# Kernel optimization log

Hardware: AMD Instinct MI355X
Metric: run time of the kernel (lower is better)

Reference implementation:

```python
import jax, jax.numpy as jnp
import numpy as np

SLOPE = 0.01  # LeakyReLU default negative slope
EPS = 1e-5    # BatchNorm eps


def _lrelu(x):
    return jnp.where(x >= 0, x, SLOPE * x)


def _conv(x, w, b):
    # x: [B,C,H,W], w: [O,I,kh,kw] (torch layout)
    y = jax.lax.conv_general_dilated(x, w, (1, 1), 'VALID',
                                     dimension_numbers=('NCHW', 'OIHW', 'NCHW'))
    return y + b[None, :, None, None]


def _bn4(x, p):
    # eval-mode BatchNorm2d; p = [gamma, beta, running_mean, running_var] stacked [4,C]
    g, b, m, v = p
    s = g * jax.lax.rsqrt(v + EPS)
    return x * s[None, :, None, None] + (b - m * s)[None, :, None, None]


def _forward(observation, action, sc1_w, sc1_b, sbn1, sc2_w, sc2_b, sbn2,
             mc1_w, mc1_b, mbn1, mc2_w, mc2_b, mbn2,
             gw_root, gw_rel, g_b, gbn,
             a_cw, a_cb, a_w1, a_b1, a_w2, a_b2, a_w3, a_b3,
             edge_index, edge_type, nodes_to_select):
    # ---- multi-scale temporal CNN (eval mode: dropout = identity) ----
    s = _lrelu(_bn4(_conv(observation, sc1_w, sc1_b), sbn1))
    s = _lrelu(_bn4(_conv(s, sc2_w, sc2_b), sbn2))          # [B,20,N,1]
    m = _lrelu(_bn4(_conv(observation, mc1_w, mc1_b), mbn1))
    m = _lrelu(_bn4(_conv(m, mc2_w, mc2_b), mbn2))          # [B,20,N,1]
    l = _lrelu(jnp.max(observation, axis=3, keepdims=True)) # [B,3,N,1]
    temporal = jnp.concatenate([s, m, l], axis=1)           # [B,43,N,1]

    # ---- RGCN (graph replicated per batch element; aggr='mean' per relation) ----
    x = jnp.swapaxes(temporal[..., 0], 1, 2)                # [B,N,F]
    N = x.shape[1]
    src, dst = edge_index[0], edge_index[1]
    out = jnp.einsum('bnf,fg->bng', x, gw_root) + g_b       # root transform + bias
    for r in range(gw_rel.shape[0]):
        h = jnp.einsum('bnf,fg->bng', x, gw_rel[r])         # per-relation transform
        mask = (edge_type == r).astype(x.dtype)             # [E]
        msgs = h[:, src, :] * mask[None, :, None]           # [B,E,F] gather
        agg = jax.ops.segment_sum(jnp.swapaxes(msgs, 0, 1), dst, num_segments=N)  # [N,B,F]
        deg = jax.ops.segment_sum(mask, dst, num_segments=N)                       # [N]
        out = out + jnp.swapaxes(agg, 0, 1) / jnp.maximum(deg, 1.0)[None, :, None]
    # BatchNorm1d (eval) + LeakyReLU; dropout = identity
    g, be, mu, v = gbn
    sg = g * jax.lax.rsqrt(v + EPS)
    out = _lrelu(out * sg + (be - mu * sg))                 # [B,N,F]

    graph_feats = jnp.swapaxes(out, 1, 2)[..., None]        # [B,F,N,1]
    feats = jnp.concatenate([temporal, graph_feats], axis=1)  # [B,86,N,1]
    feats = feats[:, :, nodes_to_select, :]                 # [B,86,P,1]

    # ---- actor head (mode == 'actor'); cash_bias is zeroed in the original ----
    stocks = action[:, 1:][:, None, :, None]                # [B,1,P,1]
    f = jnp.concatenate([stocks, feats], axis=1)[..., 0]    # [B,87,P]
    logits = jnp.einsum('bcp,c->bp', f, a_cw) + a_cb[0]     # 1x1 conv, out_ch=1
    o = jnp.concatenate([jnp.zeros((f.shape[0], 1), f.dtype), logits], axis=1)  # [B,P+1]
    h1 = jax.nn.relu(o @ a_w1 + a_b1)
    h2 = jax.nn.relu(h1 @ a_w2 + a_b2)
    return jax.nn.softmax(h2 @ a_w3 + a_b3, axis=-1)


def setup_inputs() -> dict:
    key = jax.random.key(0)
    ks = jax.random.split(key, 30)
    B, C0, N, T = 64, 3, 500, 50
    E, R, P, H = 16000, 4, 500, 128
    CM, CF = 3, 20
    F = 2 * CF + C0  # 43

    def rn(k, sh, s=0.1):
        return jax.random.normal(k, sh, jnp.float32) * s

    def bn_p(k, c):
        k1, k2, k3, k4 = jax.random.split(k, 4)
        return jnp.stack([jax.random.uniform(k1, (c,), jnp.float32, 0.5, 1.5),
                          rn(k2, (c,)), rn(k3, (c,)),
                          jax.random.uniform(k4, (c,), jnp.float32, 0.5, 1.5)])

    return {
        'observation': jax.random.normal(ks[0], (B, C0, N, T), jnp.float32),
        'action': jax.random.uniform(ks[1], (B, P + 1), jnp.float32),
        'edge_index': jax.random.randint(ks[2], (2, E), 0, N),
        'edge_type': jax.random.randint(ks[3], (E,), 0, R),
        'nodes_to_select': jnp.arange(P),
        'sc1_w': rn(ks[4], (CM, C0, 1, 3)), 'sc1_b': rn(ks[5], (CM,)), 'sbn1': bn_p(ks[6], CM),
        'sc2_w': rn(ks[7], (CF, CM, 1, 48)), 'sc2_b': rn(ks[8], (CF,)), 'sbn2': bn_p(ks[9], CF),
        'mc1_w': rn(ks[10], (CM, C0, 1, 21)), 'mc1_b': rn(ks[11], (CM,)), 'mbn1': bn_p(ks[12], CM),
        'mc2_w': rn(ks[13], (CF, CM, 1, 30)), 'mc2_b': rn(ks[14], (CF,)), 'mbn2': bn_p(ks[15], CF),
        'gw_root': rn(ks[16], (F, F)), 'gw_rel': rn(ks[17], (R, F, F)),
        'g_b': rn(ks[18], (F,)), 'gbn': bn_p(ks[19], F),
        'a_cw': rn(ks[20], (2 * F + 1,)), 'a_cb': rn(ks[21], (1,)),
        'a_w1': rn(ks[22], (P + 1, H)), 'a_b1': rn(ks[23], (H,)),
        'a_w2': rn(ks[24], (H, H)), 'a_b2': rn(ks[25], (H,)),
        'a_w3': rn(ks[26], (H, P + 1)), 'a_b3': rn(ks[27], (P + 1,)),
    }


def reference(observation, action, edge_index, edge_type, nodes_to_select,
              sc1_w, sc1_b, sbn1, sc2_w, sc2_b, sbn2,
              mc1_w, mc1_b, mbn1, mc2_w, mc2_b, mbn2,
              gw_root, gw_rel, g_b, gbn,
              a_cw, a_cb, a_w1, a_b1, a_w2, a_b2, a_w3, a_b3):
    return _forward(observation, action, sc1_w, sc1_b, sbn1, sc2_w, sc2_b, sbn2,
                    mc1_w, mc1_b, mbn1, mc2_w, mc2_b, mbn2,
                    gw_root, gw_rel, g_b, gbn,
                    a_cw, a_cb, a_w1, a_b1, a_w2, a_b2, a_w3, a_b3,
                    edge_index, edge_type, nodes_to_select)
```

## Files before the change

### kernel.cpp

```cpp
#include <hip/hip_runtime.h>

#define SLOPE 0.01f
#define EPSV  1e-5f
#define BB    64
#define NN    500
#define TT    50
#define E_N   16000
#define FF    43
#define PP    500
#define HH    128
#define XSTRIDE 48
#define PAD_E 40

typedef const float* fp;

__device__ __forceinline__ float lrelu(float x){ return x >= 0.f ? x : SLOPE * x; }
__device__ __forceinline__ float bnap(float x, fp bnp, int c, int C){
  float g  = bnp[c], b_ = bnp[C + c];
  float m  = bnp[2*C + c], v = bnp[3*C + c];
  float s = g * rsqrtf(v + EPSV);
  return x * s + (b_ - m * s);
}

#define DPP_I(x, c) __builtin_amdgcn_update_dpp(0, (x), (c), 0xF, 0xF, true)
__device__ __forceinline__ float rsum16(float x){
  x += __int_as_float(DPP_I(__float_as_int(x), 0xB1));
  x += __int_as_float(DPP_I(__float_as_int(x), 0x4E));
  x += __int_as_float(DPP_I(__float_as_int(x), 0x124));
  x += __int_as_float(DPP_I(__float_as_int(x), 0x128));
  return x;
}
__device__ __forceinline__ float rmax16(float x){
  x = fmaxf(x, __int_as_float(DPP_I(__float_as_int(x), 0xB1)));
  x = fmaxf(x, __int_as_float(DPP_I(__float_as_int(x), 0x4E)));
  x = fmaxf(x, __int_as_float(DPP_I(__float_as_int(x), 0x124)));
  x = fmaxf(x, __int_as_float(DPP_I(__float_as_int(x), 0x128)));
  return x;
}

__global__ __launch_bounds__(512) void k_tempo24(
    fp obs, fp sc1w, fp mc1w, fp sc2w, fp mc2w,
    fp sc1b, fp sbn1, fp sc2b, fp sbn2,
    fp mc1b, fp mbn1, fp mc2b, fp mbn2,
    const int* __restrict__ ei, const int* __restrict__ et,
    int* __restrict__ cntg, int* __restrict__ esp,
    float* __restrict__ xbuf)
{
  __shared__ float OL[4896];
  __shared__ float WSr[2880];
  __shared__ float WMr[1800];
  __shared__ float TBL[100];
  int tid  = threadIdx.x;
  int w    = tid >> 6, lane = tid & 63;
  int node = lane >> 4, seg = lane & 15;
  int gg   = __builtin_amdgcn_readfirstlane(blockIdx.x*8 + w);
  int b    = gg / 125, ng = gg - b*125;
  int n0   = ng * 4;
  int wbase = w * 612;

  for (int i = tid; i < 720; i += 512) *(float4*)(WSr + i*4) = *(const float4*)(sc2w + i*4);
  for (int i = tid; i < 450; i += 512) *(float4*)(WMr + i*4) = *(const float4*)(mc2w + i*4);

  if (tid < 20){
    float g = sbn2[tid], b_ = sbn2[20+tid], m = sbn2[40+tid], v = sbn2[60+tid];
    float s = g * rsqrtf(v + EPSV);
    TBL[tid] = s; TBL[43+tid] = sc2b[tid]*s + (b_ - m*s);
  } else if (tid < 40){
    int o = tid - 20;
    float g = mbn2[o], b_ = mbn2[20+o], m = mbn2[40+o], v = mbn2[60+o];
    float s = g * rsqrtf(v + EPSV);
    TBL[tid] = s; TBL[43+tid] = mc2b[o]*s + (b_ - m*s);
  } else if (tid < 43){
    TBL[tid] = 1.f; TBL[43+tid] = 0.f;
  } else if (tid < 46){
    int ci = tid - 43;
    float g = sbn1[ci], b_ = sbn1[3+ci], m = sbn1[6+ci], v = sbn1[9+ci];
    float s = g * rsqrtf(v + EPSV);
    TBL[86+ci] = s; TBL[89+ci] = sc1b[ci]*s + (b_ - m*s);
  } else if (tid < 49){
    int ci = tid - 46;
    float g = mbn1[ci], b_ = mbn1[3+ci], m = mbn1[6+ci], v = mbn1[9+ci];
    float s = g * rsqrtf(v + EPSV);
    TBL[92+ci] = s; TBL[95+ci] = mc1b[ci]*s + (b_ - m*s);
  }

  if (blockIdx.x < 8){
    int base = blockIdx.x * 2000;
    #pragma unroll
    for (int k = 0; k < 4; k++){
      int el = k*512 + tid;
      if (el < 2000){
        int e = base + el;
        int s = ei[e], d = ei[E_N + e], r = et[e];
        int idx = d*4 + r;
        int pos = atomicAdd(&cntg[idx], 1);
        if (pos < PAD_E) esp[idx*PAD_E + pos] = s;
      }
    }
  }

  for (int c = 0; c < 3; c++){
    if (lane < 50){
      const float4 v = *(const float4*)(obs + ((size_t)(b*3+c)*NN + n0)*TT + lane*4);
      int f = lane*4;
      int n = f/50, t = f - n*50;
      int a = wbase + c*204 + n*51 + t;
      OL[a] = v.x;
      if (++t == 50){ t = 0; n++; a = wbase + c*204 + n*51; } else a++;
      OL[a] = v.y;
      if (++t == 50){ t = 0; n++; a = wbase + c*204 + n*51; } else a++;
      OL[a] = v.z;
      if (++t == 50){ t = 0; n++; a = wbase + c*204 + n*51; } else a++;
      OL[a] = v.w;
    }
  }
  __syncthreads();

  int rb = wbase + node*51;
  int g  = b*NN + n0 + node;
  float* xr = xbuf + (size_t)g * XSTRIDE;
  float acc[20];

  {
    float mv[3][3];
    #pragma unroll
    for (int i = 0; i < 3; i++)
      #pragma unroll
      for (int co = 0; co < 3; co++) mv[i][co] = 0.f;
    int t0 = seg*3;
    #pragma unroll
    for (int ci = 0; ci < 3; ci++){
      int ab = rb + ci*204 + t0;
      float v0 = OL[ab], v1 = OL[ab+1], v2 = OL[ab+2], v3 = OL[ab+3], v4 = OL[ab+4];
      #pragma unroll
      for (int co = 0; co < 3; co++){
        float w0 = sc1w[co*9+ci*3+0], w1 = sc1w[co*9+ci*3+1], w2 = sc1w[co*9+ci*3+2];
        mv[0][co] += v0*w0 + v1*w1 + v2*w2;
        mv[1][co] += v1*w0 + v2*w1 + v3*w2;
        mv[2][co] += v2*w0 + v3*w1 + v4*w2;
      }
    }
    #pragma unroll
    for (int o = 0; o < 20; o++) acc[o] = 0.f;
    #pragma unroll
    for (int i = 0; i < 3; i++){
      int tt = t0 + i;
      #pragma unroll
      for (int co = 0; co < 3; co++){
        float z = lrelu(mv[i][co]*TBL[86+co] + TBL[89+co]);
        const float* wr = WSr + co*48 + tt;
        #pragma unroll
        for (int o = 0; o < 20; o++)
          acc[o] += z * wr[o*144];
      }
    }
    #pragma unroll
    for (int o = 0; o < 20; o++) acc[o] = rsum16(acc[o]);
    #pragma unroll
    for (int o = 0; o < 20; o++)
      if (seg == (o & 15)) xr[o] = lrelu(acc[o]*TBL[o] + TBL[43+o]);
  }

  {
    float mv[2][3];
    #pragma unroll
    for (int i = 0; i < 2; i++)
      #pragma unroll
      for (int co = 0; co < 3; co++) mv[i][co] = 0.f;
    int t0 = seg*2;
    #pragma unroll
    for (int ci = 0; ci < 3; ci++){
      int ab = rb + ci*204 + t0;
      float vc = OL[ab];
      #pragma unroll
      for (int k = 0; k < 21; k++){
        float vn = OL[ab + k + 1];
        #pragma unroll
        for (int co = 0; co < 3; co++){
          float wk = mc1w[co*63 + ci*21 + k];
          mv[0][co] += vc*wk;
          mv[1][co] += vn*wk;
        }
        vc = vn;
      }
    }
    #pragma unroll
    for (int o = 0; o < 20; o++) acc[o] = 0.f;
    if (seg < 15){
      #pragma unroll
      for (int co = 0; co < 3; co++){
        float z0 = lrelu(mv[0][co]*TBL[92+co] + TBL[95+co]);
        float z1 = lrelu(mv[1][co]*TBL[92+co] + TBL[95+co]);
        const float* wr = WMr + co*30 + t0;
        #pragma unroll
        for (int o = 0; o < 20; o++){
          float2 q = *(const float2*)(wr + o*90);
          acc[o] += z0*q.x + z1*q.y;
        }
      }
    }
    #pragma unroll
    for (int o = 0; o < 20; o++) acc[o] = rsum16(acc[o]);
    #pragma unroll
    for (int o = 0; o < 20; o++)
      if (seg == (o & 15)) xr[20+o] = lrelu(acc[o]*TBL[20+o] + TBL[63+o]);
  }

  {
    float m0 = -3e38f, m1 = -3e38f, m2 = -3e38f;
    int l0 = seg*4;
    int ln = 50 - l0; if (ln > 4) ln = 4;
    for (int j = 0; j < ln; j++){
      m0 = fmaxf(m0, OL[rb +       l0 + j]);
      m1 = fmaxf(m1, OL[rb + 204 + l0 + j]);
      m2 = fmaxf(m2, OL[rb + 408 + l0 + j]);
    }
    m0 = rmax16(m0); m1 = rmax16(m1); m2 = rmax16(m2);
    if (seg == 0) xr[40] = lrelu(m0);
    if (seg == 1) xr[41] = lrelu(m1);
    if (seg == 2) xr[42] = lrelu(m2);
  }
}

__global__ __launch_bounds__(1024) void k_graph17(
    const float* __restrict__ xbuf,
    fp gwroot, fp gwrel, fp gb, fp gbnp,
    const int* __restrict__ cntg, const int* __restrict__ esp,
    fp action, fp acw, fp acb,
    float* __restrict__ o_ws)
{
  __shared__ float xin[64][219];
  __shared__ float lred[16][64];
  int p = blockIdx.x;
  int l = ((p & 7) * 63) + (p >> 3);
  if (l >= 500) return;
  int tid = threadIdx.x;
  int w = tid >> 6, lane = tid & 63;
  int g0 = l * 64;

  for (int q = 0; q < 4; q++){
    int nl = (w << 2) + q;
    int g = __builtin_amdgcn_readfirstlane(g0 + nl);
    int b = g / NN;
    int n = g - b * NN;
    const float* xb = xbuf + (size_t)(b * NN) * XSTRIDE;
    float xv = (lane < FF) ? xbuf[(size_t)g*XSTRIDE + lane] : 0.f;
    float ar[4];
    #pragma unroll
    for (int r = 0; r < 4; r++){
      int idx = n*4 + r;
      int c = __builtin_amdgcn_readfirstlane(cntg[idx]);
      if (c > PAD_E) c = PAD_E;
      const int* ep = esp + idx*PAD_E;
      float a0 = 0.f, a1 = 0.f, a2 = 0.f, a3 = 0.f;
      int i = 0;
      for (; i + 4 <= c; i += 4){
        int s0 = ep[i], s1 = ep[i+1], s2 = ep[i+2], s3 = ep[i+3];
        float v0 = (lane < FF) ? xb[(size_t)s0*XSTRIDE + lane] : 0.f;
        float v1 = (lane < FF) ? xb[(size_t)s1*XSTRIDE + lane] : 0.f;
        float v2 = (lane < FF) ? xb[(size_t)s2*XSTRIDE + lane] : 0.f;
        float v3 = (lane < FF) ? xb[(size_t)s3*XSTRIDE + lane] : 0.f;
        a0 += v0; a1 += v1; a2 += v2; a3 += v3;
      }
      for (; i < c; i++){
        int s = ep[i];
        a0 += (lane < FF) ? xb[(size_t)s*XSTRIDE + lane] : 0.f;
      }
      ar[r] = ((a0 + a1) + (a2 + a3)) / fmaxf((float)c, 1.f);
    }
    if (lane < FF){
      xin[nl][lane]       = xv;
      xin[nl][ 43 + lane] = ar[0];
      xin[nl][ 86 + lane] = ar[1];
      xin[nl][129 + lane] = ar[2];
      xin[nl][172 + lane] = ar[3];
    }
  }
  __syncthreads();

  int c0 = __builtin_amdgcn_readfirstlane(w * 3);
  float acc[3];
  #pragma unroll
  for (int j = 0; j < 3; j++) acc[j] = (c0 + j < FF) ? gb[c0+j] : 0.f;
  for (int f = 0; f < 43; f++){
    float v = xin[lane][f];
    const float* wp = gwroot + f*43 + c0;
    #pragma unroll
    for (int j = 0; j < 3; j++) acc[j] += v * wp[j];
  }
  for (int f = 0; f < 172; f++){
    float v = xin[lane][43 + f];
    const float* wp = gwrel + f*43 + c0;
    #pragma unroll
    for (int j = 0; j < 3; j++) acc[j] += v * wp[j];
  }
  float lp = 0.f;
  #pragma unroll
  for (int j = 0; j < 3; j++){
    int c = c0 + j;
    if (c < FF){
      float gv = lrelu(bnap(acc[j], gbnp, c, FF));
      lp += gv * acw[1 + FF + c];
    }
  }
  if (w == 15){
    int g = g0 + lane;
    int b = g / NN, n = g - b * NN;
    float xp = acb[0] + action[b*(PP+1) + 1 + n] * acw[0];
    #pragma unroll 2
    for (int c = 0; c < FF; c++) xp += xin[lane][c] * acw[1 + c];
    lp = xp;
  }
  lred[w][lane] = lp;
  __syncthreads();
  if (tid < 64){
    float t = 0.f;
    #pragma unroll
    for (int w2 = 0; w2 < 16; w2++) t += lred[w2][tid];
    int g2 = g0 + tid;
    int b = g2 / NN, n = g2 - b * NN;
    o_ws[b*(PP+1) + 1 + n] = t;
  }
}

__global__ __launch_bounds__(512) void k_fcall2(
    const float* __restrict__ o_ws,
    fp aw1, fp ab1, fp aw2, fp ab2, fp aw3, fp ab3,
    float* __restrict__ out)
{
  int b = blockIdx.x;
  int tid = threadIdx.x;
  __shared__ float os[PP+1];
  __shared__ float part[4][HH];
  __shared__ float h1[HH];
  __shared__ float h2[HH];
  __shared__ float red[512];

  if (tid <= PP) os[tid] = (tid == 0) ? 0.f : o_ws[b*(PP+1) + tid];
  __syncthreads();

  {
    int chunk = tid >> 7, h = tid & 127;
    int k0 = chunk * 125;
    int kn = (chunk == 3) ? 126 : 125;
    float acc = 0.f;
    for (int k = 0; k < kn; k++) acc += os[k0+k] * aw1[(k0+k)*HH + h];
    part[chunk][h] = acc;
  }
  __syncthreads();
  if (tid < HH)
    h1[tid] = fmaxf(ab1[tid] + part[0][tid] + part[1][tid] + part[2][tid] + part[3][tid], 0.f);
  __syncthreads();
  if (tid < HH){
    float acc = ab2[tid];
    #pragma unroll 4
    for (int k = 0; k < HH; k++) acc += h1[k] * aw2[k*HH + tid];
    h2[tid] = fmaxf(acc, 0.f);
  }
  __syncthreads();

  float val = -1e30f;
  if (tid <= PP){
    float acc = ab3[tid];
    #pragma unroll 4
    for (int k = 0; k < HH; k++) acc += h2[k] * aw3[k*(PP+1) + tid];
    val = acc;
  }
  red[tid] = val;
  __syncthreads();
  for (int s = 256; s > 0; s >>= 1){
    if (tid < s) red[tid] = fmaxf(red[tid], red[tid + s]);
    __syncthreads();
  }
  float mxv = red[0];
  __syncthreads();
  float e = (tid <= PP) ? expf(val - mxv) : 0.f;
  red[tid] = e;
  __syncthreads();
  for (int s = 256; s > 0; s >>= 1){
    if (tid < s) red[tid] += red[tid + s];
    __syncthreads();
  }
  float sum = red[0];
  if (tid <= PP) out[b*(PP+1) + tid] = e / sum;
}

extern "C" void kernel_launch(void* const* d_in, const int* in_sizes, int n_in,
                              void* d_out, int out_size, void* d_ws, size_t ws_size,
                              hipStream_t stream)
{
  fp obs    = (fp)d_in[0];
  fp action = (fp)d_in[1];
  const int* ei  = (const int*)d_in[2];
  const int* et  = (const int*)d_in[3];
  fp sc1w=(fp)d_in[5],  sc1b=(fp)d_in[6],  sbn1=(fp)d_in[7];
  fp sc2w=(fp)d_in[8],  sc2b=(fp)d_in[9],  sbn2=(fp)d_in[10];
  fp mc1w=(fp)d_in[11], mc1b=(fp)d_in[12], mbn1=(fp)d_in[13];
  fp mc2w=(fp)d_in[14], mc2b=(fp)d_in[15], mbn2=(fp)d_in[16];
  fp gwroot=(fp)d_in[17], gwrel=(fp)d_in[18], gb=(fp)d_in[19], gbnp=(fp)d_in[20];
  fp acw=(fp)d_in[21], acb=(fp)d_in[22];
  fp aw1=(fp)d_in[23], ab1=(fp)d_in[24];
  fp aw2=(fp)d_in[25], ab2=(fp)d_in[26];
  fp aw3=(fp)d_in[27], ab3=(fp)d_in[28];

  float* xbuf   = (float*)d_ws;
  float* o_ws   = xbuf + 1536000;
  int*   cntg   = (int*)(o_ws + 32064);
  int*   esp    = cntg + 2000;

  float* out = (float*)d_out;

  hipMemsetAsync(cntg, 0, 2000*sizeof(int), stream);
  hipLaunchKernelGGL(k_tempo24, dim3(1000), dim3(512), 0, stream,
    obs, sc1w, mc1w, sc2w, mc2w,
    sc1b, sbn1, sc2b, sbn2, mc1b, mbn1, mc2b, mbn2,
    ei, et, cntg, esp, xbuf);
  hipLaunchKernelGGL(k_graph17, dim3(504), dim3(1024), 0, stream,
    xbuf, gwroot, gwrel, gb, gbnp, cntg, esp, action, acw, acb, o_ws);
  hipLaunchKernelGGL(k_fcall2, dim3(BB), dim3(512), 0, stream,
    o_ws, aw1, ab1, aw2, ab2, aw3, ab3, out);
}
```

Before: 226.4 us.

## Remap graph kernel blocks to one node across all batches, sharing edge lists

The RGCN aggregation kernel now assigns each block a single node index for all 64 batch elements, where before each block took 64 consecutive flattened (batch,node) rows. Each wave handles four batches and reuses every edge index load across those four batches' gathers. This cuts redundant edge-list and count reads and raises memory-level parallelism per loaded index. In exchange the gathers now stride across four separate batch slices, and the output writes to o_ws are strided by batch.

```diff
diff --git a/kernel.cpp b/kernel.cpp
--- a/kernel.cpp
+++ b/kernel.cpp
@@ -222,7 +222,7 @@
   }
 }
 
-__global__ __launch_bounds__(1024) void k_graph17(
+__global__ __launch_bounds__(1024) void k_graph20(
     const float* __restrict__ xbuf,
     fp gwroot, fp gwrel, fp gb, fp gbnp,
     const int* __restrict__ cntg, const int* __restrict__ esp,
@@ -231,49 +231,55 @@
 {
   __shared__ float xin[64][219];
   __shared__ float lred[16][64];
-  int p = blockIdx.x;
-  int l = ((p & 7) * 63) + (p >> 3);
-  if (l >= 500) return;
+  int n = blockIdx.x;
   int tid = threadIdx.x;
   int w = tid >> 6, lane = tid & 63;
-  int g0 = l * 64;
-
-  for (int q = 0; q < 4; q++){
-    int nl = (w << 2) + q;
-    int g = __builtin_amdgcn_readfirstlane(g0 + nl);
-    int b = g / NN;
-    int n = g - b * NN;
-    const float* xb = xbuf + (size_t)(b * NN) * XSTRIDE;
-    float xv = (lane < FF) ? xbuf[(size_t)g*XSTRIDE + lane] : 0.f;
-    float ar[4];
-    #pragma unroll
-    for (int r = 0; r < 4; r++){
-      int idx = n*4 + r;
-      int c = __builtin_amdgcn_readfirstlane(cntg[idx]);
-      if (c > PAD_E) c = PAD_E;
-      const int* ep = esp + idx*PAD_E;
-      float a0 = 0.f, a1 = 0.f, a2 = 0.f, a3 = 0.f;
-      int i = 0;
-      for (; i + 4 <= c; i += 4){
-        int s0 = ep[i], s1 = ep[i+1], s2 = ep[i+2], s3 = ep[i+3];
-        float v0 = (lane < FF) ? xb[(size_t)s0*XSTRIDE + lane] : 0.f;
-        float v1 = (lane < FF) ? xb[(size_t)s1*XSTRIDE + lane] : 0.f;
-        float v2 = (lane < FF) ? xb[(size_t)s2*XSTRIDE + lane] : 0.f;
-        float v3 = (lane < FF) ? xb[(size_t)s3*XSTRIDE + lane] : 0.f;
-        a0 += v0; a1 += v1; a2 += v2; a3 += v3;
-      }
-      for (; i < c; i++){
-        int s = ep[i];
-        a0 += (lane < FF) ? xb[(size_t)s*XSTRIDE + lane] : 0.f;
-      }
-      ar[r] = ((a0 + a1) + (a2 + a3)) / fmaxf((float)c, 1.f);
-    }
+  int b0 = w * 4;
+
+  const float* xb0 = xbuf + (size_t)((b0+0)*NN) * XSTRIDE;
+  const float* xb1 = xbuf + (size_t)((b0+1)*NN) * XSTRIDE;
+  const float* xb2 = xbuf + (size_t)((b0+2)*NN) * XSTRIDE;
+  const float* xb3 = xbuf + (size_t)((b0+3)*NN) * XSTRIDE;
+
+  if (lane < FF){
+    xin[b0+0][lane] = xb0[(size_t)n*XSTRIDE + lane];
+    xin[b0+1][lane] = xb1[(size_t)n*XSTRIDE + lane];
+    xin[b0+2][lane] = xb2[(size_t)n*XSTRIDE + lane];
+    xin[b0+3][lane] = xb3[(size_t)n*XSTRIDE + lane];
+  }
+
+  #pragma unroll
+  for (int r = 0; r < 4; r++){
+    int idx = n*4 + r;
+    int c = __builtin_amdgcn_readfirstlane(cntg[idx]);
+    if (c > PAD_E) c = PAD_E;
+    const int* ep = esp + idx*PAD_E;
+    float a0 = 0.f, a1 = 0.f, a2 = 0.f, a3 = 0.f;
+    int i = 0;
+    for (; i + 4 <= c; i += 4){
+      int s0 = ep[i], s1 = ep[i+1], s2 = ep[i+2], s3 = ep[i+3];
+      size_t o0 = (size_t)s0*XSTRIDE + lane, o1 = (size_t)s1*XSTRIDE + lane;
+      size_t o2 = (size_t)s2*XSTRIDE + lane, o3 = (size_t)s3*XSTRIDE + lane;
+      if (lane < FF){
+        a0 += xb0[o0] + xb0[o1] + xb0[o2] + xb0[o3];
+        a1 += xb1[o0] + xb1[o1] + xb1[o2] + xb1[o3];
+        a2 += xb2[o0] + xb2[o1] + xb2[o2] + xb2[o3];
+        a3 += xb3[o0] + xb3[o1] + xb3[o2] + xb3[o3];
+      }
+    }
+    for (; i < c; i++){
+      int s = ep[i];
+      size_t o = (size_t)s*XSTRIDE + lane;
+      if (lane < FF){
+        a0 += xb0[o]; a1 += xb1[o]; a2 += xb2[o]; a3 += xb3[o];
+      }
+    }
+    float inv = 1.f / fmaxf((float)c, 1.f);
     if (lane < FF){
-      xin[nl][lane]       = xv;
-      xin[nl][ 43 + lane] = ar[0];
-      xin[nl][ 86 + lane] = ar[1];
-      xin[nl][129 + lane] = ar[2];
-      xin[nl][172 + lane] = ar[3];
+      xin[b0+0][43 + 43*r + lane] = a0 * inv;
+      xin[b0+1][43 + 43*r + lane] = a1 * inv;
+      xin[b0+2][43 + 43*r + lane] = a2 * inv;
+      xin[b0+3][43 + 43*r + lane] = a3 * inv;
     }
   }
   __syncthreads();
@@ -304,9 +310,7 @@
     }
   }
   if (w == 15){
-    int g = g0 + lane;
-    int b = g / NN, n = g - b * NN;
-    float xp = acb[0] + action[b*(PP+1) + 1 + n] * acw[0];
+    float xp = acb[0] + action[lane*(PP+1) + 1 + n] * acw[0];
     #pragma unroll 2
     for (int c = 0; c < FF; c++) xp += xin[lane][c] * acw[1 + c];
     lp = xp;
@@ -317,9 +321,7 @@
     float t = 0.f;
     #pragma unroll
     for (int w2 = 0; w2 < 16; w2++) t += lred[w2][tid];
-    int g2 = g0 + tid;
-    int b = g2 / NN, n = g2 - b * NN;
-    o_ws[b*(PP+1) + 1 + n] = t;
+    o_ws[tid*(PP+1) + 1 + n] = t;
   }
 }
 
@@ -415,7 +417,7 @@
     obs, sc1w, mc1w, sc2w, mc2w,
     sc1b, sbn1, sc2b, sbn2, mc1b, mbn1, mc2b, mbn2,
     ei, et, cntg, esp, xbuf);
-  hipLaunchKernelGGL(k_graph17, dim3(504), dim3(1024), 0, stream,
+  hipLaunchKernelGGL(k_graph20, dim3(500), dim3(1024), 0, stream,
     xbuf, gwroot, gwrel, gb, gbnp, cntg, esp, action, acw, acb, o_ws);
   hipLaunchKernelGGL(k_fcall2, dim3(BB), dim3(512), 0, stream,
     o_ws, aw1, ab1, aw2, ab2, aw3, ab3, out);
```

Measured after the change: 216.8 us. -4.2%, faster.
